# Optimization experiments

Measured on AMD Instinct MI355X. Metric: run time of the kernel, lower is better.

The kernel has to match this reference:

```python
import jax, jax.numpy as jnp
import numpy as np

NUM_TOKENS = 8192
D_MODEL = 512
D_FF = 1024
NUM_EXPERTS = 8
TOP_K = 2


def setup_inputs() -> dict:
    key = jax.random.key(0)
    k_x, k_r, k_w1, k_w2 = jax.random.split(key, 4)
    x = jax.random.normal(k_x, (NUM_TOKENS, D_MODEL), dtype=jnp.float32)
    # Router weight [num_experts, d_model]
    w_router = jax.random.normal(k_r, (NUM_EXPERTS, D_MODEL), dtype=jnp.float32) * 0.02
    # Expert weights stored as [E, N, K] (kernel convention: y = x @ W.T)
    w1 = jax.random.normal(k_w1, (NUM_EXPERTS, D_FF, D_MODEL), dtype=jnp.float32) * 0.02
    w2 = jax.random.normal(k_w2, (NUM_EXPERTS, D_MODEL, D_FF), dtype=jnp.float32) * 0.02
    return {"x": x, "w_router": w_router, "w1": w1, "w2": w2}


def reference(x, w_router, w1, w2):
    # Router: softmax over experts, top-k selection, renormalized gates
    logits = jnp.einsum("td,ed->te", x, w_router)            # [T, E]
    probs = jax.nn.softmax(logits, axis=-1)
    top_vals, top_idx = jax.lax.top_k(probs, TOP_K)           # [T, k]
    top_vals = top_vals / jnp.sum(top_vals, axis=-1, keepdims=True)

    # Combine weights per (token, expert): topk weight if selected else 0.
    # out[t] = sum_e gate[t,e] * W2[e] @ silu(W1[e] @ x[t])
    out = jnp.zeros_like(x)
    for e in range(NUM_EXPERTS):
        gate_e = jnp.sum(jnp.where(top_idx == e, top_vals, 0.0), axis=-1)  # [T]
        h = jax.nn.silu(jnp.einsum("td,fd->tf", x, w1[e]))                 # [T, d_ff]
        y = jnp.einsum("tf,df->td", h, w2[e])                              # [T, d]
        out = out + gate_e[:, None] * y
    return out
```

## Files before the change

### kernel.cpp

```cpp
#include <hip/hip_runtime.h>
#include <hip/hip_bf16.h>

#define NT 8192
#define DM 512
#define DF 1024
#define NE 8
#define MAXROWS (NT*2)

typedef __bf16 bf16_8 __attribute__((ext_vector_type(8)));
typedef float  f32_4  __attribute__((ext_vector_type(4)));
typedef unsigned short us8 __attribute__((ext_vector_type(8)));

__device__ inline unsigned short f2bf(float f) {
    unsigned int u = __float_as_uint(f);
    u = u + 0x7fffu + ((u >> 16) & 1u);
    return (unsigned short)(u >> 16);
}

__device__ inline bf16_8 as_bf(us8 v) { return __builtin_bit_cast(bf16_8, v); }

__device__ inline void gld16(const unsigned short* g, unsigned short* l) {
    __builtin_amdgcn_global_load_lds(
        (const __attribute__((address_space(1))) unsigned int*)g,
        (__attribute__((address_space(3))) unsigned int*)l, 16, 0, 0);
}

__global__ __launch_bounds__(256) void cast_kernel(const float* __restrict__ in,
                                                   unsigned short* __restrict__ out,
                                                   int n4) {
    int i = blockIdx.x * 256 + threadIdx.x;
    if (i >= n4) return;
    float4 v = ((const float4*)in)[i];
    ushort4 o;
    o.x = f2bf(v.x); o.y = f2bf(v.y); o.z = f2bf(v.z); o.w = f2bf(v.w);
    ((ushort4*)out)[i] = o;
}

__global__ __launch_bounds__(256) void router_kernel(const float* __restrict__ x,
                                                     const float* __restrict__ wr,
                                                     int* __restrict__ eidx,
                                                     float2* __restrict__ gates) {
    const int wid = threadIdx.x >> 6;
    const int lane = threadIdx.x & 63;
    const int t = blockIdx.x * 4 + wid;

    const float4* xrow = (const float4*)(x + (size_t)t * DM);
    float4 xv0 = xrow[lane * 2];
    float4 xv1 = xrow[lane * 2 + 1];

    float logit[NE];
#pragma unroll
    for (int e = 0; e < NE; ++e) {
        const float4* wrow = (const float4*)(wr + (size_t)e * DM);
        float4 w0 = wrow[lane * 2];
        float4 w1v = wrow[lane * 2 + 1];
        float s = xv0.x * w0.x + xv0.y * w0.y + xv0.z * w0.z + xv0.w * w0.w
                + xv1.x * w1v.x + xv1.y * w1v.y + xv1.z * w1v.z + xv1.w * w1v.w;
#pragma unroll
        for (int off = 32; off >= 1; off >>= 1) s += __shfl_xor(s, off);
        logit[e] = s;
    }

    if (lane == 0) {
        int i0 = 0; float m0 = logit[0];
#pragma unroll
        for (int e = 1; e < NE; ++e) if (logit[e] > m0) { m0 = logit[e]; i0 = e; }
        int i1 = -1; float m1 = -1e30f;
#pragma unroll
        for (int e = 0; e < NE; ++e) if (e != i0 && logit[e] > m1) { m1 = logit[e]; i1 = e; }
        float d = expf(m1 - m0);
        float g0 = 1.0f / (1.0f + d);
        float g1 = 1.0f - g0;
        eidx[t] = i0 | (i1 << 8);
        gates[t] = make_float2(g0, g1);
    }
}

__global__ __launch_bounds__(256) void build_lists_kernel(const int* __restrict__ eidx,
                                                          const float2* __restrict__ gates,
                                                          int* __restrict__ counts,
                                                          int* __restrict__ token_list,
                                                          float* __restrict__ gate_list) {
    const int e = blockIdx.x;
    const int tid = threadIdx.x;
    const int wid = tid >> 6, lane = tid & 63;
    __shared__ int wsum[4];
    __shared__ int base;
    if (tid == 0) base = 0;
    __syncthreads();
    for (int c = 0; c < NT; c += 256) {
        int t = c + tid;
        int ei = eidx[t];
        int i0 = ei & 0xff, i1 = (ei >> 8) & 0xff;
        bool match0 = (i0 == e), match1 = (i1 == e);
        bool m = match0 || match1;
        unsigned long long mask = __ballot(m);
        if (lane == 0) wsum[wid] = __popcll(mask);
        __syncthreads();
        int pre = 0;
#pragma unroll
        for (int w = 0; w < 4; ++w) if (w < wid) pre += wsum[w];
        int tot = wsum[0] + wsum[1] + wsum[2] + wsum[3];
        if (m) {
            int pos = base + pre + __popcll(mask & ((1ULL << lane) - 1ULL));
            token_list[e * NT + pos] = t;
            float2 g = gates[t];
            gate_list[e * NT + pos] = match0 ? g.x : g.y;
        }
        __syncthreads();
        if (tid == 0) base += tot;
        __syncthreads();
    }
    if (tid == 0) counts[e] = base;
}

__global__ void scan_kernel(const int* __restrict__ counts, int* __restrict__ offsets) {
    if (threadIdx.x == 0) {
        int s = 0;
        for (int e = 0; e < NE; ++e) { offsets[e] = s; s += counts[e]; }
    }
}

template <bool G1>
__global__ __launch_bounds__(256, 4) void moe_gemm(const unsigned short* __restrict__ Abase,
                                                   const unsigned short* __restrict__ Wbase,
                                                   unsigned short* __restrict__ h_out,
                                                   float* __restrict__ out,
                                                   const int* __restrict__ counts,
                                                   const int* __restrict__ offsets,
                                                   const int* __restrict__ token_list,
                                                   const float* __restrict__ gate_list) {
    constexpr int K = G1 ? DM : DF;
    constexpr int NCOLS = G1 ? DF : DM;
    constexpr int NSTEP = K / 32;
    constexpr int TILE_E = 128 * 32;
    const int e = blockIdx.z;
    const int cnt = counts[e];
    const int row0 = blockIdx.y * 128;
    if (row0 >= cnt) return;
    const int col0 = blockIdx.x * 128;
    const int off_e = offsets[e];

    __shared__ __align__(16) unsigned short Alds[2 * TILE_E];
    __shared__ __align__(16) unsigned short Blds[2 * TILE_E];

    const int tid = threadIdx.x;
    const int wid = tid >> 6;
    const int lane = tid & 63;

    const int c0 = wid * 128 + lane;
    const int c1 = c0 + 64;
    const int r0 = c0 >> 2, q0 = c0 & 3;
    const int r1 = c1 >> 2, q1 = c1 & 3;
    const int qs0 = q0 ^ (r0 & 3);
    const int qs1 = q1 ^ (r1 & 3);

    const unsigned short* gA0;
    const unsigned short* gA1;
    {
        int rr0 = min(row0 + r0, cnt - 1);
        int rr1 = min(row0 + r1, cnt - 1);
        if (G1) {
            gA0 = Abase + (size_t)token_list[e * NT + rr0] * K + qs0 * 8;
            gA1 = Abase + (size_t)token_list[e * NT + rr1] * K + qs1 * 8;
        } else {
            gA0 = Abase + (size_t)(off_e + rr0) * K + qs0 * 8;
            gA1 = Abase + (size_t)(off_e + rr1) * K + qs1 * 8;
        }
    }
    const unsigned short* gB0 = Wbase + ((size_t)e * NCOLS + col0 + r0) * K + qs0 * 8;
    const unsigned short* gB1 = Wbase + ((size_t)e * NCOLS + col0 + r1) * K + qs1 * 8;

    const int ldsOff0 = (wid * 128) * 8;
    const int ldsOff1 = (wid * 128 + 64) * 8;

    const int wr = wid >> 1, wc = wid & 1;
    const int lrow = lane & 15;
    const int kcs = (lane >> 4) ^ (lrow & 3);
    int offA[4], offB[4];
#pragma unroll
    for (int m = 0; m < 4; ++m)
        offA[m] = (wr * 64 + m * 16 + lrow) * 32 + kcs * 8;
#pragma unroll
    for (int n = 0; n < 4; ++n)
        offB[n] = (wc * 64 + n * 16 + lrow) * 32 + kcs * 8;

    f32_4 acc[4][4];
#pragma unroll
    for (int m = 0; m < 4; ++m)
#pragma unroll
        for (int n = 0; n < 4; ++n) acc[m][n] = (f32_4){0.f, 0.f, 0.f, 0.f};

    auto issue = [&](int t) {
        int bb = t & 1;
        unsigned short* A_l = Alds + bb * TILE_E;
        unsigned short* B_l = Blds + bb * TILE_E;
        int k0 = t * 32;
        gld16(gA0 + k0, A_l + ldsOff0);
        gld16(gA1 + k0, A_l + ldsOff1);
        gld16(gB0 + k0, B_l + ldsOff0);
        gld16(gB1 + k0, B_l + ldsOff1);
    };

    issue(0);
#pragma unroll 2
    for (int t = 0; t < NSTEP; ++t) {
        if (t + 1 < NSTEP) {
            issue(t + 1);
            asm volatile("s_waitcnt vmcnt(4)" ::: "memory");
        } else {
            asm volatile("s_waitcnt vmcnt(0)" ::: "memory");
        }
        __builtin_amdgcn_sched_barrier(0);
        __builtin_amdgcn_s_barrier();

        const unsigned short* A_l = Alds + (t & 1) * TILE_E;
        const unsigned short* B_l = Blds + (t & 1) * TILE_E;
        bf16_8 a[4], b[4];
#pragma unroll
        for (int m = 0; m < 4; ++m) a[m] = as_bf(*(const us8*)(A_l + offA[m]));
#pragma unroll
        for (int n = 0; n < 4; ++n) b[n] = as_bf(*(const us8*)(B_l + offB[n]));
#pragma unroll
        for (int m = 0; m < 4; ++m)
#pragma unroll
            for (int n = 0; n < 4; ++n)
                acc[m][n] = __builtin_amdgcn_mfma_f32_16x16x32_bf16(a[m], b[n], acc[m][n], 0, 0, 0);

        asm volatile("s_waitcnt lgkmcnt(0)" ::: "memory");
        __builtin_amdgcn_sched_barrier(0);
        __builtin_amdgcn_s_barrier();
    }

#pragma unroll
    for (int m = 0; m < 4; ++m) {
#pragma unroll
        for (int n = 0; n < 4; ++n) {
#pragma unroll
            for (int q = 0; q < 4; ++q) {
                int lr = wr * 64 + m * 16 + (lane >> 4) * 4 + q;
                int lc = wc * 64 + n * 16 + (lane & 15);
                int r = row0 + lr;
                if (r < cnt) {
                    float v = acc[m][n][q];
                    if (G1) {
                        v = v / (1.0f + expf(-v));
                        h_out[(size_t)(off_e + r) * DF + col0 + lc] = f2bf(v);
                    } else {
                        float g = gate_list[e * NT + r];
                        int tok = token_list[e * NT + r];
                        atomicAdd(&out[(size_t)tok * DM + col0 + lc], g * v);
                    }
                }
            }
        }
    }
}

extern "C" void kernel_launch(void* const* d_in, const int* in_sizes, int n_in,
                              void* d_out, int out_size, void* d_ws, size_t ws_size,
                              hipStream_t stream) {
    const float* x   = (const float*)d_in[0];
    const float* wrt = (const float*)d_in[1];
    const float* w1  = (const float*)d_in[2];
    const float* w2  = (const float*)d_in[3];
    float* out = (float*)d_out;

    char* ws = (char*)d_ws;
    size_t o = 0;
    auto alloc = [&](size_t bytes) { size_t r = o; o += (bytes + 255) & ~255UL; return r; };
    unsigned short* x_bf  = (unsigned short*)(ws + alloc((size_t)NT * DM * 2));
    unsigned short* w1_bf = (unsigned short*)(ws + alloc((size_t)NE * DF * DM * 2));
    unsigned short* w2_bf = (unsigned short*)(ws + alloc((size_t)NE * DM * DF * 2));
    unsigned short* h_bf  = (unsigned short*)(ws + alloc((size_t)MAXROWS * DF * 2));
    int*   counts     = (int*)(ws + alloc(NE * 4));
    int*   offsets    = (int*)(ws + alloc(NE * 4));
    int*   token_list = (int*)(ws + alloc((size_t)NE * NT * 4));
    float* gate_list  = (float*)(ws + alloc((size_t)NE * NT * 4));
    int*   eidx       = (int*)(ws + alloc((size_t)NT * 4));
    float2* gates     = (float2*)(ws + alloc((size_t)NT * 8));

    hipMemsetAsync(out, 0, (size_t)NT * DM * 4, stream);

    int n4x = NT * DM / 4;
    cast_kernel<<<(n4x + 255) / 256, 256, 0, stream>>>(x, x_bf, n4x);
    int n4w = NE * DF * DM / 4;
    cast_kernel<<<(n4w + 255) / 256, 256, 0, stream>>>(w1, w1_bf, n4w);
    cast_kernel<<<(n4w + 255) / 256, 256, 0, stream>>>(w2, w2_bf, n4w);

    router_kernel<<<NT / 4, 256, 0, stream>>>(x, wrt, eidx, gates);
    build_lists_kernel<<<NE, 256, 0, stream>>>(eidx, gates, counts, token_list, gate_list);
    scan_kernel<<<1, 64, 0, stream>>>(counts, offsets);

    moe_gemm<true><<<dim3(DF / 128, NT / 128, NE), 256, 0, stream>>>(
        x_bf, w1_bf, h_bf, nullptr, counts, offsets, token_list, gate_list);
    moe_gemm<false><<<dim3(DM / 128, NT / 128, NE), 256, 0, stream>>>(
        h_bf, w2_bf, nullptr, out, counts, offsets, token_list, gate_list);
}
```

Baseline: 169.0 us.

## Double K-tile depth to 64 with 8-way XOR swizzle in expert GEMM

Result: slower. 190.0 us (+12.5%).

```diff
diff --git a/kernel.cpp b/kernel.cpp
--- a/kernel.cpp
+++ b/kernel.cpp
@@ -122,7 +122,7 @@
 }
 
 template <bool G1>
-__global__ __launch_bounds__(256, 4) void moe_gemm(const unsigned short* __restrict__ Abase,
+__global__ __launch_bounds__(256, 2) void moe_gemm(const unsigned short* __restrict__ Abase,
                                                    const unsigned short* __restrict__ Wbase,
                                                    unsigned short* __restrict__ h_out,
                                                    float* __restrict__ out,
@@ -132,8 +132,8 @@
                                                    const float* __restrict__ gate_list) {
     constexpr int K = G1 ? DM : DF;
     constexpr int NCOLS = G1 ? DF : DM;
-    constexpr int NSTEP = K / 32;
-    constexpr int TILE_E = 128 * 32;
+    constexpr int NSTEP = K / 64;
+    constexpr int TILE_E = 128 * 64;
     const int e = blockIdx.z;
     const int cnt = counts[e];
     const int row0 = blockIdx.y * 128;
@@ -148,42 +148,26 @@
     const int wid = tid >> 6;
     const int lane = tid & 63;
 
-    const int c0 = wid * 128 + lane;
-    const int c1 = c0 + 64;
-    const int r0 = c0 >> 2, q0 = c0 & 3;
-    const int r1 = c1 >> 2, q1 = c1 & 3;
-    const int qs0 = q0 ^ (r0 & 3);
-    const int qs1 = q1 ^ (r1 & 3);
-
-    const unsigned short* gA0;
-    const unsigned short* gA1;
-    {
-        int rr0 = min(row0 + r0, cnt - 1);
-        int rr1 = min(row0 + r1, cnt - 1);
+    const int g_oct = (lane & 7) ^ (lane >> 3);
+    const unsigned short* gA[4];
+    const unsigned short* gB[4];
+    int ldsOff[4];
+#pragma unroll
+    for (int j = 0; j < 4; ++j) {
+        int row_j = wid * 32 + j * 8 + (lane >> 3);
+        int rr = min(row0 + row_j, cnt - 1);
         if (G1) {
-            gA0 = Abase + (size_t)token_list[e * NT + rr0] * K + qs0 * 8;
-            gA1 = Abase + (size_t)token_list[e * NT + rr1] * K + qs1 * 8;
+            gA[j] = Abase + (size_t)token_list[e * NT + rr] * K + g_oct * 8;
         } else {
-            gA0 = Abase + (size_t)(off_e + rr0) * K + qs0 * 8;
-            gA1 = Abase + (size_t)(off_e + rr1) * K + qs1 * 8;
-        }
-    }
-    const unsigned short* gB0 = Wbase + ((size_t)e * NCOLS + col0 + r0) * K + qs0 * 8;
-    const unsigned short* gB1 = Wbase + ((size_t)e * NCOLS + col0 + r1) * K + qs1 * 8;
-
-    const int ldsOff0 = (wid * 128) * 8;
-    const int ldsOff1 = (wid * 128 + 64) * 8;
+            gA[j] = Abase + (size_t)(off_e + rr) * K + g_oct * 8;
+        }
+        gB[j] = Wbase + ((size_t)e * NCOLS + col0 + row_j) * K + g_oct * 8;
+        ldsOff[j] = (wid * 256 + j * 64) * 8;
+    }
 
     const int wr = wid >> 1, wc = wid & 1;
     const int lrow = lane & 15;
-    const int kcs = (lane >> 4) ^ (lrow & 3);
-    int offA[4], offB[4];
-#pragma unroll
-    for (int m = 0; m < 4; ++m)
-        offA[m] = (wr * 64 + m * 16 + lrow) * 32 + kcs * 8;
-#pragma unroll
-    for (int n = 0; n < 4; ++n)
-        offB[n] = (wc * 64 + n * 16 + lrow) * 32 + kcs * 8;
+    const int kc = lane >> 4;
 
     f32_4 acc[4][4];
 #pragma unroll
@@ -195,19 +179,19 @@
         int bb = t & 1;
         unsigned short* A_l = Alds + bb * TILE_E;
         unsigned short* B_l = Blds + bb * TILE_E;
-        int k0 = t * 32;
-        gld16(gA0 + k0, A_l + ldsOff0);
-        gld16(gA1 + k0, A_l + ldsOff1);
-        gld16(gB0 + k0, B_l + ldsOff0);
-        gld16(gB1 + k0, B_l + ldsOff1);
+        int k0 = t * 64;
+#pragma unroll
+        for (int j = 0; j < 4; ++j) {
+            gld16(gA[j] + k0, A_l + ldsOff[j]);
+            gld16(gB[j] + k0, B_l + ldsOff[j]);
+        }
     };
 
     issue(0);
-#pragma unroll 2
     for (int t = 0; t < NSTEP; ++t) {
         if (t + 1 < NSTEP) {
             issue(t + 1);
-            asm volatile("s_waitcnt vmcnt(4)" ::: "memory");
+            asm volatile("s_waitcnt vmcnt(8)" ::: "memory");
         } else {
             asm volatile("s_waitcnt vmcnt(0)" ::: "memory");
         }
@@ -216,16 +200,27 @@
 
         const unsigned short* A_l = Alds + (t & 1) * TILE_E;
         const unsigned short* B_l = Blds + (t & 1) * TILE_E;
-        bf16_8 a[4], b[4];
-#pragma unroll
-        for (int m = 0; m < 4; ++m) a[m] = as_bf(*(const us8*)(A_l + offA[m]));
-#pragma unroll
-        for (int n = 0; n < 4; ++n) b[n] = as_bf(*(const us8*)(B_l + offB[n]));
-#pragma unroll
-        for (int m = 0; m < 4; ++m)
-#pragma unroll
-            for (int n = 0; n < 4; ++n)
-                acc[m][n] = __builtin_amdgcn_mfma_f32_16x16x32_bf16(a[m], b[n], acc[m][n], 0, 0, 0);
+#pragma unroll
+        for (int s = 0; s < 2; ++s) {
+            bf16_8 a[4], b[4];
+#pragma unroll
+            for (int m = 0; m < 4; ++m) {
+                int row = wr * 64 + m * 16 + lrow;
+                int oct = (s * 4 + kc) ^ (lrow & 7);
+                a[m] = as_bf(*(const us8*)(A_l + row * 64 + oct * 8));
+            }
+#pragma unroll
+            for (int n = 0; n < 4; ++n) {
+                int row = wc * 64 + n * 16 + lrow;
+                int oct = (s * 4 + kc) ^ (lrow & 7);
+                b[n] = as_bf(*(const us8*)(B_l + row * 64 + oct * 8));
+            }
+#pragma unroll
+            for (int m = 0; m < 4; ++m)
+#pragma unroll
+                for (int n = 0; n < 4; ++n)
+                    acc[m][n] = __builtin_amdgcn_mfma_f32_16x16x32_bf16(a[m], b[n], acc[m][n], 0, 0, 0);
+        }
 
         asm volatile("s_waitcnt lgkmcnt(0)" ::: "memory");
         __builtin_amdgcn_sched_barrier(0);
```

## Compact expert tile list and deepen GEMM load pipeline to four stages

Applied to the files above, without the earlier changes.

Measured after the change: 210.0 us. 24.3% more time.

```diff
diff --git a/kernel.cpp b/kernel.cpp
--- a/kernel.cpp
+++ b/kernel.cpp
@@ -6,6 +6,7 @@
 #define DF 1024
 #define NE 8
 #define MAXROWS (NT*2)
+#define MAXTILES 144
 
 typedef __bf16 bf16_8 __attribute__((ext_vector_type(8)));
 typedef float  f32_4  __attribute__((ext_vector_type(4)));
@@ -114,35 +115,48 @@
     if (tid == 0) counts[e] = base;
 }
 
-__global__ void scan_kernel(const int* __restrict__ counts, int* __restrict__ offsets) {
+__global__ void scan_kernel(const int* __restrict__ counts, int* __restrict__ offsets,
+                            int* __restrict__ tile_e, int* __restrict__ tile_r0,
+                            int* __restrict__ ntiles) {
     if (threadIdx.x == 0) {
-        int s = 0;
-        for (int e = 0; e < NE; ++e) { offsets[e] = s; s += counts[e]; }
+        int s = 0, nt = 0;
+        for (int e = 0; e < NE; ++e) {
+            offsets[e] = s;
+            int c = counts[e];
+            for (int r0 = 0; r0 < c; r0 += 128) { tile_e[nt] = e; tile_r0[nt] = r0; ++nt; }
+            s += c;
+        }
+        *ntiles = nt;
     }
 }
 
 template <bool G1>
-__global__ __launch_bounds__(256, 4) void moe_gemm(const unsigned short* __restrict__ Abase,
+__global__ __launch_bounds__(256, 2) void moe_gemm(const unsigned short* __restrict__ Abase,
                                                    const unsigned short* __restrict__ Wbase,
                                                    unsigned short* __restrict__ h_out,
                                                    float* __restrict__ out,
                                                    const int* __restrict__ counts,
                                                    const int* __restrict__ offsets,
                                                    const int* __restrict__ token_list,
-                                                   const float* __restrict__ gate_list) {
+                                                   const float* __restrict__ gate_list,
+                                                   const int* __restrict__ tile_e,
+                                                   const int* __restrict__ tile_r0,
+                                                   const int* __restrict__ ntiles) {
     constexpr int K = G1 ? DM : DF;
     constexpr int NCOLS = G1 ? DF : DM;
     constexpr int NSTEP = K / 32;
     constexpr int TILE_E = 128 * 32;
-    const int e = blockIdx.z;
+
+    const int tl = blockIdx.y;
+    if (tl >= *ntiles) return;
+    const int e = tile_e[tl];
+    const int row0 = tile_r0[tl];
     const int cnt = counts[e];
-    const int row0 = blockIdx.y * 128;
-    if (row0 >= cnt) return;
     const int col0 = blockIdx.x * 128;
     const int off_e = offsets[e];
 
-    __shared__ __align__(16) unsigned short Alds[2 * TILE_E];
-    __shared__ __align__(16) unsigned short Blds[2 * TILE_E];
+    __shared__ __align__(16) unsigned short Alds[4 * TILE_E];
+    __shared__ __align__(16) unsigned short Blds[4 * TILE_E];
 
     const int tid = threadIdx.x;
     const int wid = tid >> 6;
@@ -192,7 +206,7 @@
         for (int n = 0; n < 4; ++n) acc[m][n] = (f32_4){0.f, 0.f, 0.f, 0.f};
 
     auto issue = [&](int t) {
-        int bb = t & 1;
+        int bb = t & 3;
         unsigned short* A_l = Alds + bb * TILE_E;
         unsigned short* B_l = Blds + bb * TILE_E;
         int k0 = t * 32;
@@ -202,20 +216,9 @@
         gld16(gB1 + k0, B_l + ldsOff1);
     };
 
-    issue(0);
-#pragma unroll 2
-    for (int t = 0; t < NSTEP; ++t) {
-        if (t + 1 < NSTEP) {
-            issue(t + 1);
-            asm volatile("s_waitcnt vmcnt(4)" ::: "memory");
-        } else {
-            asm volatile("s_waitcnt vmcnt(0)" ::: "memory");
-        }
-        __builtin_amdgcn_sched_barrier(0);
-        __builtin_amdgcn_s_barrier();
-
-        const unsigned short* A_l = Alds + (t & 1) * TILE_E;
-        const unsigned short* B_l = Blds + (t & 1) * TILE_E;
+    auto compute = [&](int t) {
+        const unsigned short* A_l = Alds + (t & 3) * TILE_E;
+        const unsigned short* B_l = Blds + (t & 3) * TILE_E;
         bf16_8 a[4], b[4];
 #pragma unroll
         for (int m = 0; m < 4; ++m) a[m] = as_bf(*(const us8*)(A_l + offA[m]));
@@ -226,11 +229,26 @@
 #pragma unroll
             for (int n = 0; n < 4; ++n)
                 acc[m][n] = __builtin_amdgcn_mfma_f32_16x16x32_bf16(a[m], b[n], acc[m][n], 0, 0, 0);
-
         asm volatile("s_waitcnt lgkmcnt(0)" ::: "memory");
         __builtin_amdgcn_sched_barrier(0);
         __builtin_amdgcn_s_barrier();
-    }
+    };
+
+#define VMWAIT(n) do { \
+        asm volatile("s_waitcnt vmcnt(" #n ")" ::: "memory"); \
+        __builtin_amdgcn_sched_barrier(0); \
+        __builtin_amdgcn_s_barrier(); } while (0)
+
+    issue(0); issue(1); issue(2);
+    for (int t = 0; t < NSTEP - 3; ++t) {
+        issue(t + 3);
+        VMWAIT(12);
+        compute(t);
+    }
+    VMWAIT(8);  compute(NSTEP - 3);
+    VMWAIT(4);  compute(NSTEP - 2);
+    VMWAIT(0);  compute(NSTEP - 1);
+#undef VMWAIT
 
 #pragma unroll
     for (int m = 0; m < 4; ++m) {
@@ -279,6 +297,9 @@
     float* gate_list  = (float*)(ws + alloc((size_t)NE * NT * 4));
     int*   eidx       = (int*)(ws + alloc((size_t)NT * 4));
     float2* gates     = (float2*)(ws + alloc((size_t)NT * 8));
+    int*   tile_e     = (int*)(ws + alloc(MAXTILES * 4));
+    int*   tile_r0    = (int*)(ws + alloc(MAXTILES * 4));
+    int*   ntiles     = (int*)(ws + alloc(4));
 
     hipMemsetAsync(out, 0, (size_t)NT * DM * 4, stream);
 
@@ -290,10 +311,12 @@
 
     router_kernel<<<NT / 4, 256, 0, stream>>>(x, wrt, eidx, gates);
     build_lists_kernel<<<NE, 256, 0, stream>>>(eidx, gates, counts, token_list, gate_list);
-    scan_kernel<<<1, 64, 0, stream>>>(counts, offsets);
-
-    moe_gemm<true><<<dim3(DF / 128, NT / 128, NE), 256, 0, stream>>>(
-        x_bf, w1_bf, h_bf, nullptr, counts, offsets, token_list, gate_list);
-    moe_gemm<false><<<dim3(DM / 128, NT / 128, NE), 256, 0, stream>>>(
-        h_bf, w2_bf, nullptr, out, counts, offsets, token_list, gate_list);
-}
+    scan_kernel<<<1, 64, 0, stream>>>(counts, offsets, tile_e, tile_r0, ntiles);
+
+    moe_gemm<true><<<dim3(DF / 128, 136, 1), 256, 0, stream>>>(
+        x_bf, w1_bf, h_bf, nullptr, counts, offsets, token_list, gate_list,
+        tile_e, tile_r0, ntiles);
+    moe_gemm<false><<<dim3(DM / 128, 136, 1), 256, 0, stream>>>(
+        h_bf, w2_bf, nullptr, out, counts, offsets, token_list, gate_list,
+        tile_e, tile_r0, ntiles);
+}
```
